# Kernel optimization log

Hardware: AMD Instinct MI355X
Metric: run time of the kernel (lower is better)

Reference implementation:

```python
import jax, jax.numpy as jnp
import numpy as np

B, S, D = 4, 1024, 1024
H = 16
HD = D // H  # 64
LN_EPS = 1e-5


def setup_inputs() -> dict:
    key = jax.random.key(0)
    ks = jax.random.split(key, 12)
    s = 1.0 / np.sqrt(D)
    return {
        "x": jax.random.normal(ks[0], (B, S, D), dtype=jnp.float32),
        "wq": jax.random.normal(ks[1], (D, D), dtype=jnp.float32) * s,
        "bq": jnp.zeros((D,), dtype=jnp.float32),
        "wk": jax.random.normal(ks[2], (D, D), dtype=jnp.float32) * s,
        "bk": jnp.zeros((D,), dtype=jnp.float32),
        "wv": jax.random.normal(ks[3], (D, D), dtype=jnp.float32) * s,
        "bv": jnp.zeros((D,), dtype=jnp.float32),
        "wl": jax.random.normal(ks[4], (D, D), dtype=jnp.float32) * s,
        "bl": jnp.zeros((D,), dtype=jnp.float32),
        "ln_g": jnp.ones((D,), dtype=jnp.float32),
        "ln_b": jnp.zeros((D,), dtype=jnp.float32),
    }


def _heads(t):
    # [B,S,D] -> [B,H,S,HD]
    return t.reshape(B, S, H, HD).transpose(0, 2, 1, 3)


def reference(x, wq, bq, wk, bk, wv, bv, wl, bl, ln_g, ln_b):
    q = _heads(x @ wq.T + bq)
    k = _heads(x @ wk.T + bk)
    v = _heads(x @ wv.T + bv)
    score = jnp.einsum("bhqd,bhkd->bhqk", q, k)
    # NOTE: unusual order — softmax first, THEN divide by sqrt(head_size)
    score = jax.nn.softmax(score, axis=-1) / jnp.sqrt(jnp.float32(HD))
    att = jnp.einsum("bhqk,bhkd->bhqd", score, v)
    att = att.transpose(0, 2, 1, 3).reshape(B, S, D)
    # residual added BEFORE the output linear
    y = (att + x) @ wl.T + bl
    # LayerNorm over last dim
    mu = jnp.mean(y, axis=-1, keepdims=True)
    var = jnp.mean(jnp.square(y - mu), axis=-1, keepdims=True)
    out = (y - mu) * jax.lax.rsqrt(var + LN_EPS) * ln_g + ln_b
    # dropout is identity in eval mode
    return out
```

## Files before the change

kernel.cpp:

```cpp
#include <hip/hip_runtime.h>
#include <cstdint>
#include <cstddef>

typedef __bf16 bf16;
typedef __bf16 bf16x4_t __attribute__((ext_vector_type(4)));
typedef __bf16 bf16x8_t __attribute__((ext_vector_type(8)));
typedef float f32x4_t __attribute__((ext_vector_type(4)));

#define DEV static __device__ __forceinline__

DEV void gload16(const void* g, void* l) {
  __builtin_amdgcn_global_load_lds((const __attribute__((address_space(1))) void*)g,
                                   (__attribute__((address_space(3))) void*)l, 16, 0, 0);
}

DEV f32x4_t mfma16(bf16x8_t a, bf16x8_t b, f32x4_t c) {
  return __builtin_amdgcn_mfma_f32_16x16x32_bf16(a, b, c, 0, 0, 0);
}

#define BAR __builtin_amdgcn_s_barrier()
#define FENCE asm volatile("" ::: "memory")
#define VMC(n) asm volatile("s_waitcnt vmcnt(" #n ")" ::: "memory")

__global__ __launch_bounds__(256) void k_convert(
    const float* __restrict__ x, const float* __restrict__ wq,
    const float* __restrict__ wk, const float* __restrict__ wv,
    const float* __restrict__ wl,
    bf16* __restrict__ xb, bf16* __restrict__ wqkvb, bf16* __restrict__ wlb) {
  const size_t M1 = (size_t)1 << 20;
  size_t i = ((size_t)blockIdx.x * 256 + threadIdx.x) * 4;
  const float* src; bf16* dst; size_t off;
  if (i < 4 * M1)      { src = x;  dst = xb;           off = i; }
  else if (i < 5 * M1) { src = wq; dst = wqkvb;        off = i - 4 * M1; }
  else if (i < 6 * M1) { src = wk; dst = wqkvb + M1;   off = i - 5 * M1; }
  else if (i < 7 * M1) { src = wv; dst = wqkvb + 2*M1; off = i - 6 * M1; }
  else                 { src = wl; dst = wlb;          off = i - 7 * M1; }
  f32x4_t v = *(const f32x4_t*)&src[off];
  bf16x4_t o;
  o[0] = (bf16)v[0]; o[1] = (bf16)v[1]; o[2] = (bf16)v[2]; o[3] = (bf16)v[3];
  *(bf16x4_t*)&dst[off] = o;
}

__global__ __launch_bounds__(256) void k_gemm_qkv(
    const bf16* __restrict__ W, const bf16* __restrict__ Xb,
    const float* __restrict__ bq, const float* __restrict__ bk,
    const float* __restrict__ bv,
    bf16* __restrict__ Q, bf16* __restrict__ Kc, bf16* __restrict__ VT) {
  __shared__ alignas(16) bf16 smem[16384];
  bf16* lA = smem;
  bf16* lB = smem + 8192;
  const int tid = threadIdx.x, wave = tid >> 6, lane = tid & 63;
  const int wm = (wave >> 1) * 64, wn = (wave & 1) * 64;
  const int fr = lane & 15, fg = lane >> 4;
  const int csw = (((lane & 7) ^ (lane >> 3)) << 3);
  const int m0 = blockIdx.x * 128, n0 = blockIdx.y * 128;

  f32x4_t acc[4][4];
  const f32x4_t vzero = {0.f, 0.f, 0.f, 0.f};
#pragma unroll
  for (int a = 0; a < 4; ++a)
#pragma unroll
    for (int c = 0; c < 4; ++c) acc[a][c] = vzero;

  const int rowoff = wave * 8 + (lane >> 3);

  for (int kt = 0; kt < 16; ++kt) {
#pragma unroll
    for (int i = 0; i < 4; ++i) {
      gload16(W + (size_t)(m0 + i * 32 + rowoff) * 1024 + kt * 64 + csw,
              &lA[(i * 32 + wave * 8) * 64]);
      gload16(Xb + (size_t)(n0 + i * 32 + rowoff) * 1024 + kt * 64 + csw,
              &lB[(i * 32 + wave * 8) * 64]);
    }
    __syncthreads();
    bf16x8_t af[4][2], bfr[4][2];
#pragma unroll
    for (int mi = 0; mi < 4; ++mi)
#pragma unroll
      for (int ks = 0; ks < 2; ++ks) {
        const int r = wm + mi * 16 + fr;
        af[mi][ks] = *(const bf16x8_t*)
            &lA[r * 64 + ((((ks << 2) + fg) ^ (fr & 7)) << 3)];
      }
#pragma unroll
    for (int ni = 0; ni < 4; ++ni)
#pragma unroll
      for (int ks = 0; ks < 2; ++ks) {
        const int r = wn + ni * 16 + fr;
        bfr[ni][ks] = *(const bf16x8_t*)
            &lB[r * 64 + ((((ks << 2) + fg) ^ (fr & 7)) << 3)];
      }
    __builtin_amdgcn_s_setprio(1);
#pragma unroll
    for (int ks = 0; ks < 2; ++ks)
#pragma unroll
      for (int mi = 0; mi < 4; ++mi)
#pragma unroll
        for (int ni = 0; ni < 4; ++ni)
          acc[mi][ni] = mfma16(af[mi][ks], bfr[ni][ks], acc[mi][ni]);
    __builtin_amdgcn_s_setprio(0);
    __syncthreads();
  }

  const int region = m0 >> 10;
  const float* bp = (region == 0) ? bq : ((region == 1) ? bk : bv);
  if (region < 2) {
    bf16* QK = (region == 0) ? Q : Kc;
#pragma unroll
    for (int mi = 0; mi < 4; ++mi) {
      const int f = (m0 & 1023) + wm + mi * 16 + fg * 4;
      const int h = f >> 6, d = f & 63;
#pragma unroll
      for (int ni = 0; ni < 4; ++ni) {
        const int t = n0 + wn + ni * 16 + fr;
        const int b = t >> 10, s = t & 1023;
        const int bh = b * 16 + h;
        f32x4_t v = acc[mi][ni];
        bf16x4_t o;
#pragma unroll
        for (int j = 0; j < 4; ++j) o[j] = (bf16)(v[j] + bp[f + j]);
        *(bf16x4_t*)&QK[((size_t)bh * 1024 + s) * 64 + d] = o;
      }
    }
  } else {
#pragma unroll
    for (int mi = 0; mi < 4; ++mi) {
      const int dl = wm + mi * 16 + fg * 4;
      const int floc = (m0 & 1023) + dl;
#pragma unroll
      for (int ni = 0; ni < 4; ++ni) {
        const int sl = wn + ni * 16 + fr;
        f32x4_t v = acc[mi][ni];
#pragma unroll
        for (int j = 0; j < 4; ++j) {
          const int d = dl + j;
          smem[d * 128 + (sl ^ ((d & 7) << 3))] = (bf16)(v[j] + bp[floc + j]);
        }
      }
    }
    __syncthreads();
    const int b = n0 >> 10;
#pragma unroll
    for (int i = 0; i < 8; ++i) {
      const int d = i * 16 + (tid >> 4);
      const int c = tid & 15;
      bf16x8_t vv = *(const bf16x8_t*)&smem[d * 128 + ((c ^ (d & 7)) << 3)];
      const int floc = (m0 & 1023) + d;
      const int h = floc >> 6, dd = floc & 63;
      const int sg = (n0 & 1023) + c * 8;
      *(bf16x8_t*)&VT[((size_t)(b * 16 + h) * 64 + dd) * 1024 + sg] = vv;
    }
  }
}

DEV void gemm_mainloop(const bf16* __restrict__ A, const bf16* __restrict__ B,
                       int m0, int n0,
                       bf16 (*lA)[128 * 64], bf16 (*lB)[128 * 64],
                       f32x4_t (&acc)[4][4]) {
  const int tid = threadIdx.x, wave = tid >> 6, lane = tid & 63;
  const int wm = (wave >> 1) * 64, wn = (wave & 1) * 64;
  const int fr = lane & 15, fg = lane >> 4;
  const int rowoff = wave * 8 + (lane >> 3);
  const int csw = (((lane & 7) ^ (lane >> 3)) << 3);

  auto STAGE = [&](int buf, int kt) {
#pragma unroll
    for (int i = 0; i < 4; ++i) {
      gload16(A + (size_t)(m0 + i * 32 + rowoff) * 1024 + kt * 64 + csw,
              &lA[buf][(i * 32 + wave * 8) * 64]);
      gload16(B + (size_t)(n0 + i * 32 + rowoff) * 1024 + kt * 64 + csw,
              &lB[buf][(i * 32 + wave * 8) * 64]);
    }
  };

  auto COMPUTE = [&](int buf) {
    bf16x8_t af[4][2], bfr[4][2];
#pragma unroll
    for (int mi = 0; mi < 4; ++mi)
#pragma unroll
      for (int ks = 0; ks < 2; ++ks) {
        const int r = wm + mi * 16 + fr;
        af[mi][ks] = *(const bf16x8_t*)
            &lA[buf][r * 64 + ((((ks << 2) + fg) ^ (fr & 7)) << 3)];
      }
#pragma unroll
    for (int ni = 0; ni < 4; ++ni)
#pragma unroll
      for (int ks = 0; ks < 2; ++ks) {
        const int r = wn + ni * 16 + fr;
        bfr[ni][ks] = *(const bf16x8_t*)
            &lB[buf][r * 64 + ((((ks << 2) + fg) ^ (fr & 7)) << 3)];
      }
    __builtin_amdgcn_s_setprio(1);
#pragma unroll
    for (int ks = 0; ks < 2; ++ks)
#pragma unroll
      for (int mi = 0; mi < 4; ++mi)
#pragma unroll
        for (int ni = 0; ni < 4; ++ni)
          acc[mi][ni] = mfma16(af[mi][ks], bfr[ni][ks], acc[mi][ni]);
    __builtin_amdgcn_s_setprio(0);
  };

  STAGE(0, 0);
  STAGE(1, 1);
  for (int t = 0; t < 15; ++t) {
    asm volatile("s_waitcnt vmcnt(8)" ::: "memory");
    __builtin_amdgcn_s_barrier();
    COMPUTE(t & 1);
    __builtin_amdgcn_s_barrier();
    if (t < 14) STAGE(t & 1, t + 2);
  }
  asm volatile("s_waitcnt vmcnt(0)" ::: "memory");
  __builtin_amdgcn_s_barrier();
  COMPUTE(1);
}

#define P_STRIDE 72

__global__ __launch_bounds__(256) void k_attn(
    const bf16* __restrict__ Q, const bf16* __restrict__ K,
    const bf16* __restrict__ VT, const float* __restrict__ X,
    bf16* __restrict__ ATTB) {
  __shared__ alignas(16) bf16 lK[2][64 * 64];
  __shared__ alignas(16) bf16 lV[2][64 * 64];
  __shared__ alignas(16) bf16 lP[4][32 * P_STRIDE];
  const int tid = threadIdx.x, wave = tid >> 6, lane = tid & 63;
  const int bh = blockIdx.x, qt = blockIdx.y;
  const int q0 = qt * 128 + wave * 32;
  const int fr = lane & 15, fg = lane >> 4;
  const int rx = (fr & 7) << 3;
  const f32x4_t vzero = {0.f, 0.f, 0.f, 0.f};

  bf16x8_t qf[2][2];
#pragma unroll
  for (int mi = 0; mi < 2; ++mi)
#pragma unroll
    for (int ks = 0; ks < 2; ++ks)
      qf[mi][ks] = *(const bf16x8_t*)
          &Q[((size_t)bh * 1024 + q0 + mi * 16 + fr) * 64 + ks * 32 + fg * 8];

  f32x4_t oacc[2][4];
  f32x4_t lsum[2];
#pragma unroll
  for (int mi = 0; mi < 2; ++mi) {
    lsum[mi] = vzero;
#pragma unroll
    for (int dj = 0; dj < 4; ++dj) oacc[mi][dj] = vzero;
  }

  const int srow = lane >> 3;
  const int scolsw = (((lane & 7) ^ srow) * 8);

  auto STAGE = [&](int buf, int kv) {
#pragma unroll
    for (int i = 0; i < 2; ++i) {
      const int c = wave * 2 + i;
      gload16(&K[((size_t)bh * 1024 + kv * 64 + c * 8 + srow) * 64 + scolsw],
              &lK[buf][c * 512]);
      gload16(&VT[((size_t)bh * 64 + c * 8 + srow) * 1024 + kv * 64 + scolsw],
              &lV[buf][c * 512]);
    }
  };

  auto TILE = [&](int cur) {
    bf16x8_t kb[4][2];
#pragma unroll
    for (int nj = 0; nj < 4; ++nj)
#pragma unroll
      for (int ks = 0; ks < 2; ++ks) {
        const int r = nj * 16 + fr;
        kb[nj][ks] = *(const bf16x8_t*)&lK[cur][r * 64 + ((ks * 32 + fg * 8) ^ rx)];
      }
    f32x4_t s[2][4];
#pragma unroll
    for (int mi = 0; mi < 2; ++mi)
#pragma unroll
      for (int nj = 0; nj < 4; ++nj) {
        f32x4_t z = vzero;
#pragma unroll
        for (int ks = 0; ks < 2; ++ks) z = mfma16(qf[mi][ks], kb[nj][ks], z);
        s[mi][nj] = z;
      }

#pragma unroll
    for (int mi = 0; mi < 2; ++mi)
#pragma unroll
      for (int nj = 0; nj < 4; ++nj)
#pragma unroll
        for (int j = 0; j < 4; ++j) {
          float p = __expf(s[mi][nj][j]);
          lsum[mi][j] += p;
          lP[wave][(mi * 16 + fg * 4 + j) * P_STRIDE + nj * 16 + fr] = (bf16)p;
        }

    bf16x8_t vb[4][2], pa[2][2];
#pragma unroll
    for (int dj = 0; dj < 4; ++dj)
#pragma unroll
      for (int ks = 0; ks < 2; ++ks) {
        const int r = dj * 16 + fr;
        vb[dj][ks] = *(const bf16x8_t*)&lV[cur][r * 64 + ((ks * 32 + fg * 8) ^ rx)];
      }
#pragma unroll
    for (int mi = 0; mi < 2; ++mi)
#pragma unroll
      for (int ks = 0; ks < 2; ++ks)
        pa[mi][ks] = *(const bf16x8_t*)
            &lP[wave][(mi * 16 + fr) * P_STRIDE + ks * 32 + fg * 8];
#pragma unroll
    for (int mi = 0; mi < 2; ++mi)
#pragma unroll
      for (int dj = 0; dj < 4; ++dj)
#pragma unroll
        for (int ks = 0; ks < 2; ++ks)
          oacc[mi][dj] = mfma16(pa[mi][ks], vb[dj][ks], oacc[mi][dj]);
  };

  STAGE(0, 0);
  STAGE(1, 1);
  for (int kv = 0; kv < 15; ++kv) {
    VMC(4); BAR; FENCE;
    TILE(kv & 1);
    BAR; FENCE;
    if (kv < 14) STAGE(kv & 1, kv + 2);
  }
  VMC(0); BAR; FENCE;
  TILE(1);

#pragma unroll
  for (int mi = 0; mi < 2; ++mi)
#pragma unroll
    for (int m = 1; m < 16; m <<= 1)
#pragma unroll
      for (int j = 0; j < 4; ++j)
        lsum[mi][j] += __shfl_xor(lsum[mi][j], m);

  const int b = bh >> 4, h = bh & 15;
#pragma unroll
  for (int mi = 0; mi < 2; ++mi)
#pragma unroll
    for (int dj = 0; dj < 4; ++dj)
#pragma unroll
      for (int j = 0; j < 4; ++j) {
        const int s_ = q0 + mi * 16 + fg * 4 + j;
        const int d_ = dj * 16 + fr;
        const size_t tok = (size_t)b * 1024 + s_;
        const size_t fidx = (size_t)h * 64 + d_;
        float val = oacc[mi][dj][j] / lsum[mi][j] * 0.125f + X[tok * 1024 + fidx];
        ATTB[tok * 1024 + fidx] = (bf16)val;
      }
}

__global__ __launch_bounds__(256, 2) void k_gemm_out(
    const bf16* __restrict__ Wl, const bf16* __restrict__ Ax,
    const float* __restrict__ bl, float* __restrict__ Y) {
  __shared__ alignas(16) bf16 lA[2][128 * 64];
  __shared__ alignas(16) bf16 lB[2][128 * 64];
  const f32x4_t vzero = {0.f, 0.f, 0.f, 0.f};
  f32x4_t acc[4][4];
#pragma unroll
  for (int a = 0; a < 4; ++a)
#pragma unroll
    for (int c = 0; c < 4; ++c) acc[a][c] = vzero;
  const int m0 = blockIdx.x * 128, n0 = blockIdx.y * 128;
  gemm_mainloop(Wl, Ax, m0, n0, lA, lB, acc);

  const int tid = threadIdx.x, wave = tid >> 6, lane = tid & 63;
  const int wm = (wave >> 1) * 64, wn = (wave & 1) * 64;
  const int fr = lane & 15, fg = lane >> 4;
#pragma unroll
  for (int mi = 0; mi < 4; ++mi) {
    const int f = m0 + wm + mi * 16 + fg * 4;
#pragma unroll
    for (int ni = 0; ni < 4; ++ni) {
      const int t = n0 + wn + ni * 16 + fr;
      f32x4_t v = acc[mi][ni], o;
#pragma unroll
      for (int j = 0; j < 4; ++j) o[j] = v[j] + bl[f + j];
      *(f32x4_t*)&Y[(size_t)t * 1024 + f] = o;
    }
  }
}

__global__ __launch_bounds__(256) void k_ln(
    const float* __restrict__ Y, const float* __restrict__ g,
    const float* __restrict__ bta, float* __restrict__ OUT) {
  const int row = blockIdx.x, tid = threadIdx.x;
  const float* y = Y + (size_t)row * 1024;
  f32x4_t v = *(const f32x4_t*)&y[tid * 4];
  float s = v[0] + v[1] + v[2] + v[3];
  float s2 = v[0]*v[0] + v[1]*v[1] + v[2]*v[2] + v[3]*v[3];
#pragma unroll
  for (int m = 1; m < 64; m <<= 1) {
    s += __shfl_xor(s, m);
    s2 += __shfl_xor(s2, m);
  }
  __shared__ float ps[4], ps2[4];
  const int wave = tid >> 6, lane = tid & 63;
  if (lane == 0) { ps[wave] = s; ps2[wave] = s2; }
  __syncthreads();
  s = ps[0] + ps[1] + ps[2] + ps[3];
  s2 = ps2[0] + ps2[1] + ps2[2] + ps2[3];
  const float mu = s * (1.f / 1024.f);
  const float var = s2 * (1.f / 1024.f) - mu * mu;
  const float rs = rsqrtf(var + 1e-5f);
  f32x4_t gg = *(const f32x4_t*)&g[tid * 4];
  f32x4_t bb = *(const f32x4_t*)&bta[tid * 4];
  f32x4_t o;
#pragma unroll
  for (int j = 0; j < 4; ++j) o[j] = (v[j] - mu) * rs * gg[j] + bb[j];
  *(f32x4_t*)&OUT[(size_t)row * 1024 + tid * 4] = o;
}

extern "C" void kernel_launch(void* const* d_in, const int* in_sizes, int n_in,
                              void* d_out, int out_size, void* d_ws, size_t ws_size,
                              hipStream_t stream) {
  (void)in_sizes; (void)n_in; (void)out_size; (void)ws_size;
  const float* x   = (const float*)d_in[0];
  const float* wq  = (const float*)d_in[1];
  const float* bq  = (const float*)d_in[2];
  const float* wk  = (const float*)d_in[3];
  const float* bk  = (const float*)d_in[4];
  const float* wv  = (const float*)d_in[5];
  const float* bv  = (const float*)d_in[6];
  const float* wl  = (const float*)d_in[7];
  const float* bl  = (const float*)d_in[8];
  const float* lng = (const float*)d_in[9];
  const float* lnb = (const float*)d_in[10];

  const size_t MB = (size_t)1 << 20;
  char* ws = (char*)d_ws;
  bf16* xb    = (bf16*)(ws);
  bf16* wqkvb = (bf16*)(ws + 8 * MB);
  bf16* wlb   = (bf16*)(ws + 14 * MB);
  bf16* Qb    = (bf16*)(ws + 16 * MB);
  bf16* Kb    = (bf16*)(ws + 24 * MB);
  bf16* VTb   = (bf16*)(ws + 32 * MB);
  bf16* attb  = (bf16*)(ws + 40 * MB);
  float* Y    = (float*)(ws + 16 * MB);

  k_convert<<<dim3(8192), dim3(256), 0, stream>>>(x, wq, wk, wv, wl, xb, wqkvb, wlb);
  k_gemm_qkv<<<dim3(24, 32), dim3(256), 0, stream>>>(wqkvb, xb, bq, bk, bv, Qb, Kb, VTb);
  k_attn<<<dim3(64, 8), dim3(256), 0, stream>>>(Qb, Kb, VTb, x, attb);
  k_gemm_out<<<dim3(8, 32), dim3(256), 0, stream>>>(wlb, attb, bl, Y);
  k_ln<<<dim3(4096), dim3(256), 0, stream>>>(Y, lng, lnb, (float*)d_out);
}
```

Before: 113.1 us.

## Load K and V fragments directly from global memory in attention kernel

Removes the double-buffered LDS staging of K and V tiles, including the async global-to-LDS loads, the waitcnt and barriers, and has each wave read its MFMA operand fragments straight from global memory each iteration. The goal is to drop block-wide synchronisation and LDS traffic and to raise occupancy by shrinking shared memory. In exchange each of the four waves separately re-reads the same K/V tiles through the caches, and the loads are no longer prefetched ahead of compute, so latency may be exposed.

```diff
diff --git a/kernel.cpp b/kernel.cpp
--- a/kernel.cpp
+++ b/kernel.cpp
@@ -222,14 +222,11 @@
     const bf16* __restrict__ Q, const bf16* __restrict__ K,
     const bf16* __restrict__ VT, const float* __restrict__ X,
     bf16* __restrict__ ATTB) {
-  __shared__ alignas(16) bf16 lK[2][64 * 64];
-  __shared__ alignas(16) bf16 lV[2][64 * 64];
   __shared__ alignas(16) bf16 lP[4][32 * P_STRIDE];
   const int tid = threadIdx.x, wave = tid >> 6, lane = tid & 63;
   const int bh = blockIdx.x, qt = blockIdx.y;
   const int q0 = qt * 128 + wave * 32;
   const int fr = lane & 15, fg = lane >> 4;
-  const int rx = (fr & 7) << 3;
   const f32x4_t vzero = {0.f, 0.f, 0.f, 0.f};
 
   bf16x8_t qf[2][2];
@@ -249,29 +246,18 @@
     for (int dj = 0; dj < 4; ++dj) oacc[mi][dj] = vzero;
   }
 
-  const int srow = lane >> 3;
-  const int scolsw = (((lane & 7) ^ srow) * 8);
-
-  auto STAGE = [&](int buf, int kv) {
-#pragma unroll
-    for (int i = 0; i < 2; ++i) {
-      const int c = wave * 2 + i;
-      gload16(&K[((size_t)bh * 1024 + kv * 64 + c * 8 + srow) * 64 + scolsw],
-              &lK[buf][c * 512]);
-      gload16(&VT[((size_t)bh * 64 + c * 8 + srow) * 1024 + kv * 64 + scolsw],
-              &lV[buf][c * 512]);
-    }
-  };
-
-  auto TILE = [&](int cur) {
+  const bf16* Kb = K + (size_t)bh * 65536;
+  const bf16* Vb = VT + (size_t)bh * 65536;
+
+  for (int kv = 0; kv < 16; ++kv) {
     bf16x8_t kb[4][2];
 #pragma unroll
     for (int nj = 0; nj < 4; ++nj)
 #pragma unroll
-      for (int ks = 0; ks < 2; ++ks) {
-        const int r = nj * 16 + fr;
-        kb[nj][ks] = *(const bf16x8_t*)&lK[cur][r * 64 + ((ks * 32 + fg * 8) ^ rx)];
-      }
+      for (int ks = 0; ks < 2; ++ks)
+        kb[nj][ks] = *(const bf16x8_t*)
+            &Kb[(size_t)(kv * 64 + nj * 16 + fr) * 64 + ks * 32 + fg * 8];
+
     f32x4_t s[2][4];
 #pragma unroll
     for (int mi = 0; mi < 2; ++mi)
@@ -282,6 +268,14 @@
         for (int ks = 0; ks < 2; ++ks) z = mfma16(qf[mi][ks], kb[nj][ks], z);
         s[mi][nj] = z;
       }
+
+    bf16x8_t vb[4][2];
+#pragma unroll
+    for (int dj = 0; dj < 4; ++dj)
+#pragma unroll
+      for (int ks = 0; ks < 2; ++ks)
+        vb[dj][ks] = *(const bf16x8_t*)
+            &Vb[(size_t)(dj * 16 + fr) * 1024 + kv * 64 + ks * 32 + fg * 8];
 
 #pragma unroll
     for (int mi = 0; mi < 2; ++mi)
@@ -294,14 +288,7 @@
           lP[wave][(mi * 16 + fg * 4 + j) * P_STRIDE + nj * 16 + fr] = (bf16)p;
         }
 
-    bf16x8_t vb[4][2], pa[2][2];
-#pragma unroll
-    for (int dj = 0; dj < 4; ++dj)
-#pragma unroll
-      for (int ks = 0; ks < 2; ++ks) {
-        const int r = dj * 16 + fr;
-        vb[dj][ks] = *(const bf16x8_t*)&lV[cur][r * 64 + ((ks * 32 + fg * 8) ^ rx)];
-      }
+    bf16x8_t pa[2][2];
 #pragma unroll
     for (int mi = 0; mi < 2; ++mi)
 #pragma unroll
@@ -315,18 +302,7 @@
 #pragma unroll
         for (int ks = 0; ks < 2; ++ks)
           oacc[mi][dj] = mfma16(pa[mi][ks], vb[dj][ks], oacc[mi][dj]);
-  };
-
-  STAGE(0, 0);
-  STAGE(1, 1);
-  for (int kv = 0; kv < 15; ++kv) {
-    VMC(4); BAR; FENCE;
-    TILE(kv & 1);
-    BAR; FENCE;
-    if (kv < 14) STAGE(kv & 1, kv + 2);
-  }
-  VMC(0); BAR; FENCE;
-  TILE(1);
+  }
 
 #pragma unroll
   for (int mi = 0; mi < 2; ++mi)
```

Result: slower. 140.7 us (+24.3%).

## Keep attention probabilities in registers by computing transposed scores

Applied to the files above, without the earlier changes.

Computes S^T by swapping the MFMA operands, so each lane's accumulator outputs already sit in the A-operand layout needed for the P·V MFMA. This removes the per-wave LDS round trip for P (the stores, the reloads and the lP buffer). V fragments are now gathered as two 4-element LDS reads with a swizzle remap so they match the permuted k ordering. Row sums become per-lane scalars, combined by cross-lane shuffles at the end. The cost is more, smaller LDS reads for V and extra shuffle work in the epilogue.

```diff
diff --git a/kernel.cpp b/kernel.cpp
--- a/kernel.cpp
+++ b/kernel.cpp
@@ -216,15 +216,12 @@
   COMPUTE(1);
 }
 
-#define P_STRIDE 72
-
 __global__ __launch_bounds__(256) void k_attn(
     const bf16* __restrict__ Q, const bf16* __restrict__ K,
     const bf16* __restrict__ VT, const float* __restrict__ X,
     bf16* __restrict__ ATTB) {
   __shared__ alignas(16) bf16 lK[2][64 * 64];
   __shared__ alignas(16) bf16 lV[2][64 * 64];
-  __shared__ alignas(16) bf16 lP[4][32 * P_STRIDE];
   const int tid = threadIdx.x, wave = tid >> 6, lane = tid & 63;
   const int bh = blockIdx.x, qt = blockIdx.y;
   const int q0 = qt * 128 + wave * 32;
@@ -234,20 +231,18 @@
 
   bf16x8_t qf[2][2];
 #pragma unroll
-  for (int mi = 0; mi < 2; ++mi)
+  for (int qi = 0; qi < 2; ++qi)
 #pragma unroll
     for (int ks = 0; ks < 2; ++ks)
-      qf[mi][ks] = *(const bf16x8_t*)
-          &Q[((size_t)bh * 1024 + q0 + mi * 16 + fr) * 64 + ks * 32 + fg * 8];
+      qf[qi][ks] = *(const bf16x8_t*)
+          &Q[((size_t)bh * 1024 + q0 + qi * 16 + fr) * 64 + ks * 32 + fg * 8];
 
   f32x4_t oacc[2][4];
-  f32x4_t lsum[2];
-#pragma unroll
-  for (int mi = 0; mi < 2; ++mi) {
-    lsum[mi] = vzero;
-#pragma unroll
-    for (int dj = 0; dj < 4; ++dj) oacc[mi][dj] = vzero;
-  }
+  float lsum[2] = {0.f, 0.f};
+#pragma unroll
+  for (int qi = 0; qi < 2; ++qi)
+#pragma unroll
+    for (int dj = 0; dj < 4; ++dj) oacc[qi][dj] = vzero;
 
   const int srow = lane >> 3;
   const int scolsw = (((lane & 7) ^ srow) * 8);
@@ -266,55 +261,65 @@
   auto TILE = [&](int cur) {
     bf16x8_t kb[4][2];
 #pragma unroll
-    for (int nj = 0; nj < 4; ++nj)
-#pragma unroll
-      for (int ks = 0; ks < 2; ++ks) {
-        const int r = nj * 16 + fr;
-        kb[nj][ks] = *(const bf16x8_t*)&lK[cur][r * 64 + ((ks * 32 + fg * 8) ^ rx)];
+    for (int kj = 0; kj < 4; ++kj)
+#pragma unroll
+      for (int ks = 0; ks < 2; ++ks) {
+        const int r = kj * 16 + fr;
+        kb[kj][ks] = *(const bf16x8_t*)&lK[cur][r * 64 + ((ks * 32 + fg * 8) ^ rx)];
       }
     f32x4_t s[2][4];
 #pragma unroll
-    for (int mi = 0; mi < 2; ++mi)
-#pragma unroll
-      for (int nj = 0; nj < 4; ++nj) {
+    for (int qi = 0; qi < 2; ++qi)
+#pragma unroll
+      for (int kj = 0; kj < 4; ++kj) {
         f32x4_t z = vzero;
 #pragma unroll
-        for (int ks = 0; ks < 2; ++ks) z = mfma16(qf[mi][ks], kb[nj][ks], z);
-        s[mi][nj] = z;
-      }
-
-#pragma unroll
-    for (int mi = 0; mi < 2; ++mi)
-#pragma unroll
-      for (int nj = 0; nj < 4; ++nj)
-#pragma unroll
-        for (int j = 0; j < 4; ++j) {
-          float p = __expf(s[mi][nj][j]);
-          lsum[mi][j] += p;
-          lP[wave][(mi * 16 + fg * 4 + j) * P_STRIDE + nj * 16 + fr] = (bf16)p;
-        }
-
-    bf16x8_t vb[4][2], pa[2][2];
+        for (int ks = 0; ks < 2; ++ks) z = mfma16(kb[kj][ks], qf[qi][ks], z);
+        s[qi][kj] = z;
+      }
+
+    bf16x8_t vb[4][2];
 #pragma unroll
     for (int dj = 0; dj < 4; ++dj)
 #pragma unroll
       for (int ks = 0; ks < 2; ++ks) {
         const int r = dj * 16 + fr;
-        vb[dj][ks] = *(const bf16x8_t*)&lV[cur][r * 64 + ((ks * 32 + fg * 8) ^ rx)];
-      }
-#pragma unroll
-    for (int mi = 0; mi < 2; ++mi)
-#pragma unroll
-      for (int ks = 0; ks < 2; ++ks)
-        pa[mi][ks] = *(const bf16x8_t*)
-            &lP[wave][(mi * 16 + fr) * P_STRIDE + ks * 32 + fg * 8];
-#pragma unroll
-    for (int mi = 0; mi < 2; ++mi)
+        const int c0 = ks * 32 + fg * 4;
+        const int e0 = (c0 & 7) | ((((c0 >> 3) ^ (r & 7))) << 3);
+        const int c1 = c0 + 16;
+        const int e1 = (c1 & 7) | ((((c1 >> 3) ^ (r & 7))) << 3);
+        bf16x4_t lo = *(const bf16x4_t*)&lV[cur][r * 64 + e0];
+        bf16x4_t hi = *(const bf16x4_t*)&lV[cur][r * 64 + e1];
+        bf16x8_t vv;
+#pragma unroll
+        for (int j = 0; j < 4; ++j) { vv[j] = lo[j]; vv[4 + j] = hi[j]; }
+        vb[dj][ks] = vv;
+      }
+
+    bf16x8_t paf[2][2];
+#pragma unroll
+    for (int qi = 0; qi < 2; ++qi)
+#pragma unroll
+      for (int ks = 0; ks < 2; ++ks) {
+        bf16x8_t pv;
+#pragma unroll
+        for (int h = 0; h < 2; ++h)
+#pragma unroll
+          for (int j = 0; j < 4; ++j) {
+            float p = __expf(s[qi][2 * ks + h][j]);
+            lsum[qi] += p;
+            pv[h * 4 + j] = (bf16)p;
+          }
+        paf[qi][ks] = pv;
+      }
+
+#pragma unroll
+    for (int qi = 0; qi < 2; ++qi)
 #pragma unroll
       for (int dj = 0; dj < 4; ++dj)
 #pragma unroll
         for (int ks = 0; ks < 2; ++ks)
-          oacc[mi][dj] = mfma16(pa[mi][ks], vb[dj][ks], oacc[mi][dj]);
+          oacc[qi][dj] = mfma16(paf[qi][ks], vb[dj][ks], oacc[qi][dj]);
   };
 
   STAGE(0, 0);
@@ -329,25 +334,29 @@
   TILE(1);
 
 #pragma unroll
-  for (int mi = 0; mi < 2; ++mi)
-#pragma unroll
-    for (int m = 1; m < 16; m <<= 1)
-#pragma unroll
-      for (int j = 0; j < 4; ++j)
-        lsum[mi][j] += __shfl_xor(lsum[mi][j], m);
+  for (int qi = 0; qi < 2; ++qi) {
+    lsum[qi] += __shfl_xor(lsum[qi], 16);
+    lsum[qi] += __shfl_xor(lsum[qi], 32);
+  }
+  float rs[2][4];
+#pragma unroll
+  for (int qi = 0; qi < 2; ++qi)
+#pragma unroll
+    for (int j = 0; j < 4; ++j)
+      rs[qi][j] = __shfl(lsum[qi], fg * 4 + j);
 
   const int b = bh >> 4, h = bh & 15;
 #pragma unroll
-  for (int mi = 0; mi < 2; ++mi)
+  for (int qi = 0; qi < 2; ++qi)
 #pragma unroll
     for (int dj = 0; dj < 4; ++dj)
 #pragma unroll
       for (int j = 0; j < 4; ++j) {
-        const int s_ = q0 + mi * 16 + fg * 4 + j;
+        const int s_ = q0 + qi * 16 + fg * 4 + j;
         const int d_ = dj * 16 + fr;
         const size_t tok = (size_t)b * 1024 + s_;
         const size_t fidx = (size_t)h * 64 + d_;
-        float val = oacc[mi][dj][j] / lsum[mi][j] * 0.125f + X[tok * 1024 + fidx];
+        float val = oacc[qi][dj][j] / rs[qi][j] * 0.125f + X[tok * 1024 + fidx];
         ATTB[tok * 1024 + fidx] = (bf16)val;
       }
 }
```

Result: faster. 106.6 us (-5.7%).
